# Performance work log

Hardware: AMD Instinct MI355X
Metric: run time of the kernel (lower is better)

Reference implementation:

```python
import jax, jax.numpy as jnp
import numpy as np
from jax import lax

BN_EPS = 1e-5


def _gate(x, w, g, b, m, v):
    """ZPool -> 7x7 conv (2->1 ch) -> BN (eval) -> sigmoid -> multiply. x: [B,C,H,W]."""
    z = jnp.concatenate(
        [x.max(axis=1, keepdims=True), x.mean(axis=1, keepdims=True)], axis=1
    )  # [B,2,H,W]
    y = lax.conv_general_dilated(
        z, w, window_strides=(1, 1), padding=((3, 3), (3, 3)),
        dimension_numbers=("NCHW", "OIHW", "NCHW"),
    )  # [B,1,H,W]
    y = (y - m) * lax.rsqrt(v + BN_EPS) * g + b
    return x * jax.nn.sigmoid(y)


def setup_inputs() -> dict:
    key = jax.random.key(0)
    ks = jax.random.split(key, 4)
    B, C, H, W = 32, 256, 56, 56
    return {
        "x": jax.random.normal(ks[0], (B, C, H, W), dtype=jnp.float32),
        "w_ch": jax.random.normal(ks[1], (1, 2, 7, 7), dtype=jnp.float32),
        "w_cw": jax.random.normal(ks[2], (1, 2, 7, 7), dtype=jnp.float32),
        "w_hw": jax.random.normal(ks[3], (1, 2, 7, 7), dtype=jnp.float32),
        "gamma": jnp.ones((3,), jnp.float32),
        "beta": jnp.zeros((3,), jnp.float32),
        "mean": jnp.zeros((3,), jnp.float32),
        "var": jnp.ones((3,), jnp.float32),
    }


def reference(x, w_ch, w_cw, w_hw, gamma, beta, mean, var):
    # Branch 1: swap C<->H -> gate -> swap back
    x_ch = jnp.transpose(x, (0, 2, 1, 3))
    x_ch = jnp.transpose(_gate(x_ch, w_ch, gamma[0], beta[0], mean[0], var[0]), (0, 2, 1, 3))
    # Branch 2: swap C<->W -> gate -> swap back
    x_cw = jnp.transpose(x, (0, 3, 2, 1))
    x_cw = jnp.transpose(_gate(x_cw, w_cw, gamma[1], beta[1], mean[1], var[1]), (0, 3, 2, 1))
    # Branch 3: identity spatial gate
    x_hw = _gate(x, w_hw, gamma[2], beta[2], mean[2], var[2])
    return (x_ch + x_cw + x_hw) / 3.0
```

## Files before the change

kernel.cpp:

```cpp
#include <hip/hip_runtime.h>
#include <math.h>


#define B_ 32
#define C_ 256
#define H_ 56
#define W_ 56
#define HW_ 3136
#define LDSW 60
#define CG 8
#define NGRP (C_ / CG)

__device__ __forceinline__ float4 f4max(float4 a, float4 b) {
    return make_float4(fmaxf(a.x, b.x), fmaxf(a.y, b.y), fmaxf(a.z, b.z), fmaxf(a.w, b.w));
}
__device__ __forceinline__ float4 f4add(float4 a, float4 b) {
    return make_float4(a.x + b.x, a.y + b.y, a.z + b.z, a.w + b.w);
}

__global__ __launch_bounds__(256) void pool_fused(const float* __restrict__ x,
                                                  float* __restrict__ P1,
                                                  float* __restrict__ P2,
                                                  float* __restrict__ P3p) {
    __shared__ float smem[H_ * LDSW];
    const int t = threadIdx.x;
    const int b = blockIdx.x >> 5;
    const int g = blockIdx.x & (NGRP - 1);
    const int c0 = g * CG;
    const float* __restrict__ base = x + (size_t)(b * C_ + c0) * HW_;

    const int s0 = t, s1i = t + 256, s2i = t + 512, s3i = t + 768;
    const int h0 = s0 / 14,  ad0 = h0 * LDSW + (s0 - h0 * 14) * 4;
    const int h1 = s1i / 14, ad1 = h1 * LDSW + (s1i - h1 * 14) * 4;
    const int h2 = s2i / 14, ad2 = h2 * LDSW + (s2i - h2 * 14) * 4;
    const int h3 = s3i / 14, ad3 = h3 * LDSW + (s3i - h3 * 14) * 4;

    float4 mx0, mx1, mx2, mx3, su0, su1, su2, su3;
    mx0 = mx1 = mx2 = mx3 = make_float4(-INFINITY, -INFINITY, -INFINITY, -INFINITY);
    su0 = su1 = su2 = su3 = make_float4(0.f, 0.f, 0.f, 0.f);

    const float4* bp = (const float4*)base;
    float4 cur0 = bp[s0], cur1 = bp[s1i], cur2 = bp[s2i];
    float4 cur3 = (t < 16) ? bp[s3i] : make_float4(0, 0, 0, 0);

    for (int cc = 0; cc < CG; ++cc) {
        float4 nx0, nx1, nx2, nx3;
        if (cc < CG - 1) {
            const float4* nb = (const float4*)(base + (size_t)(cc + 1) * HW_);
            nx0 = nb[s0]; nx1 = nb[s1i]; nx2 = nb[s2i];
            if (t < 16) nx3 = nb[s3i];
        }
        *(float4*)&smem[ad0] = cur0;
        *(float4*)&smem[ad1] = cur1;
        *(float4*)&smem[ad2] = cur2;
        if (t < 16) *(float4*)&smem[ad3] = cur3;
        mx0 = f4max(mx0, cur0); su0 = f4add(su0, cur0);
        mx1 = f4max(mx1, cur1); su1 = f4add(su1, cur1);
        mx2 = f4max(mx2, cur2); su2 = f4add(su2, cur2);
        if (t < 16) { mx3 = f4max(mx3, cur3); su3 = f4add(su3, cur3); }
        __syncthreads();

        const int c = c0 + cc;
        if (t < 224) {
            const int q = t & 3;
            {
                const int h = t >> 2;
                float m = -INFINITY, s = 0.f;
#pragma unroll
                for (int j = 0; j < 14; ++j) {
                    float v = smem[h * LDSW + q + 4 * j];
                    m = fmaxf(m, v); s += v;
                }
                m = fmaxf(m, __shfl_down(m, 1)); s += __shfl_down(s, 1);
                m = fmaxf(m, __shfl_down(m, 2)); s += __shfl_down(s, 2);
                if (q == 0) {
                    P2[(((size_t)b * 2 + 0) * H_ + h) * C_ + c] = m;
                    P2[(((size_t)b * 2 + 1) * H_ + h) * C_ + c] = s * (1.f / 56.f);
                }
            }
            {
                const int w = t >> 2;
                float m = -INFINITY, s = 0.f;
#pragma unroll
                for (int j = 0; j < 14; ++j) {
                    float v = smem[(q * 14 + j) * LDSW + w];
                    m = fmaxf(m, v); s += v;
                }
                m = fmaxf(m, __shfl_down(m, 1)); s += __shfl_down(s, 1);
                m = fmaxf(m, __shfl_down(m, 2)); s += __shfl_down(s, 2);
                if (q == 0) {
                    P1[(((size_t)b * 2 + 0) * C_ + c) * W_ + w] = m;
                    P1[(((size_t)b * 2 + 1) * C_ + c) * W_ + w] = s * (1.f / 56.f);
                }
            }
        }
        __syncthreads();
        if (cc < CG - 1) {
            cur0 = nx0; cur1 = nx1; cur2 = nx2;
            if (t < 16) cur3 = nx3;
        }
    }
    float4* Pm = (float4*)(P3p + ((size_t)(b * NGRP + g) * 2 + 0) * HW_);
    float4* Ps = (float4*)(P3p + ((size_t)(b * NGRP + g) * 2 + 1) * HW_);
    Pm[s0] = mx0; Pm[s1i] = mx1; Pm[s2i] = mx2;
    Ps[s0] = su0; Ps[s1i] = su1; Ps[s2i] = su2;
    if (t < 16) { Pm[s3i] = mx3; Ps[s3i] = su3; }
}

__global__ __launch_bounds__(256) void combine_p3(const float* __restrict__ P3p,
                                                  float* __restrict__ P3) {
    const int idx = blockIdx.x * 256 + threadIdx.x;
    const int b = idx / HW_;
    const int hw = idx - b * HW_;
    const float* src = P3p + (size_t)b * NGRP * 2 * HW_ + hw;
    float m = -INFINITY, s = 0.f;
#pragma unroll
    for (int gg = 0; gg < NGRP; ++gg) {
        m = fmaxf(m, src[(size_t)(2 * gg + 0) * HW_]);
        s += src[(size_t)(2 * gg + 1) * HW_];
    }
    P3[((size_t)b * 2 + 0) * HW_ + hw] = m;
    P3[((size_t)b * 2 + 1) * HW_ + hw] = s * (1.f / 256.f);
}

__global__ __launch_bounds__(256) void conv_all(const float* __restrict__ P1,
                                                const float* __restrict__ P2,
                                                const float* __restrict__ P3,
                                                const float* __restrict__ w_ch,
                                                const float* __restrict__ w_cw,
                                                const float* __restrict__ w_hw,
                                                const float* __restrict__ gamma,
                                                const float* __restrict__ beta,
                                                const float* __restrict__ mean,
                                                const float* __restrict__ var,
                                                float* __restrict__ s1,
                                                float* __restrict__ s2,
                                                float* __restrict__ s3) {
    const int k = blockIdx.z;
    const float* Z; const float* wsrc; float* S; int A, D;
    if (k == 0)      { Z = P1; wsrc = w_ch; S = s1; A = C_; D = W_; }
    else if (k == 1) { Z = P2; wsrc = w_cw; S = s2; A = H_; D = C_; }
    else             { Z = P3; wsrc = w_hw; S = s3; A = H_; D = W_; }

    __shared__ float wl[98];
    const int t = threadIdx.x;
    if (t < 98) wl[t] = wsrc[t];
    __syncthreads();

    const int b = blockIdx.y;
    const int AD = A * D;
    const int idx = blockIdx.x * 256 + t;
    if (idx >= AD) return;
    const int a = idx / D;
    const int d = idx - a * D;

    const float* Z0 = Z + (size_t)b * 2 * AD;
    float acc = 0.f;
#pragma unroll
    for (int dy = 0; dy < 7; ++dy) {
        int aa = a + dy - 3;
        if (aa < 0 || aa >= A) continue;
#pragma unroll
        for (int dx = 0; dx < 7; ++dx) {
            int dd = d + dx - 3;
            if (dd < 0 || dd >= D) continue;
            acc += Z0[aa * D + dd] * wl[dy * 7 + dx]
                 + Z0[AD + aa * D + dd] * wl[49 + dy * 7 + dx];
        }
    }
    float y = (acc - mean[k]) * rsqrtf(var[k] + 1e-5f) * gamma[k] + beta[k];
    S[(size_t)b * AD + idx] = 1.f / (1.f + expf(-y));
}

__global__ __launch_bounds__(256) void final_mul(const float* __restrict__ x,
                                                 const float* __restrict__ s1,
                                                 const float* __restrict__ s2,
                                                 const float* __restrict__ s3,
                                                 float* __restrict__ out) {
    const int vid = blockIdx.x * 256 + threadIdx.x;
    const int p = vid / 784;
    const int r = vid - p * 784;
    const int h = r / 14;
    const int w4 = (r - h * 14) << 2;
    const int b = p >> 8;
    const int c = p & 255;

    const size_t xoff = (size_t)p * HW_ + h * 56 + w4;
    const float4 xv = *(const float4*)(x + xoff);
    const float4 s1v = *(const float4*)(s1 + ((size_t)(b * C_ + c)) * W_ + w4);
    const float s2s = s2[((size_t)b * H_ + h) * C_ + c];
    const float4 s3v = *(const float4*)(s3 + ((size_t)b * H_ + h) * W_ + w4);

    float4 o;
    o.x = xv.x * (s1v.x + s2s + s3v.x) * (1.f / 3.f);
    o.y = xv.y * (s1v.y + s2s + s3v.y) * (1.f / 3.f);
    o.z = xv.z * (s1v.z + s2s + s3v.z) * (1.f / 3.f);
    o.w = xv.w * (s1v.w + s2s + s3v.w) * (1.f / 3.f);
    *(float4*)(out + xoff) = o;
}

extern "C" void kernel_launch(void* const* d_in, const int* in_sizes, int n_in,
                              void* d_out, int out_size, void* d_ws, size_t ws_size,
                              hipStream_t stream) {
    const float* x = (const float*)d_in[0];
    const float* w_ch = (const float*)d_in[1];
    const float* w_cw = (const float*)d_in[2];
    const float* w_hw = (const float*)d_in[3];
    const float* gamma = (const float*)d_in[4];
    const float* beta = (const float*)d_in[5];
    const float* mean = (const float*)d_in[6];
    const float* var = (const float*)d_in[7];
    float* out = (float*)d_out;

    float* ws = (float*)d_ws;
    float* P1 = ws;
    float* P2 = P1 + 917504;
    float* P3p = P2 + 917504;
    float* P3 = P3p + 6422528;
    float* s1 = P3 + 200704;
    float* s2 = s1 + 458752;
    float* s3 = s2 + 458752;

    pool_fused<<<B_ * NGRP, 256, 0, stream>>>(x, P1, P2, P3p);
    combine_p3<<<(B_ * HW_) / 256, 256, 0, stream>>>(P3p, P3);
    conv_all<<<dim3(56, B_, 3), 256, 0, stream>>>(P1, P2, P3, w_ch, w_cw, w_hw,
                                                  gamma, beta, mean, var, s1, s2, s3);
    final_mul<<<(B_ * C_ * HW_) / 4 / 256, 256, 0, stream>>>(x, s1, s2, s3, out);
}
```

Before: 265.6 us.

## Fuse channel-partial combine into conv kernel and double channel group size

```diff
diff --git a/kernel.cpp b/kernel.cpp
--- a/kernel.cpp
+++ b/kernel.cpp
@@ -8,7 +8,7 @@
 #define W_ 56
 #define HW_ 3136
 #define LDSW 60
-#define CG 8
+#define CG 16
 #define NGRP (C_ / CG)
 
 __device__ __forceinline__ float4 f4max(float4 a, float4 b) {
@@ -24,7 +24,7 @@
                                                   float* __restrict__ P3p) {
     __shared__ float smem[H_ * LDSW];
     const int t = threadIdx.x;
-    const int b = blockIdx.x >> 5;
+    const int b = blockIdx.x >> 4;
     const int g = blockIdx.x & (NGRP - 1);
     const int c0 = g * CG;
     const float* __restrict__ base = x + (size_t)(b * C_ + c0) * HW_;
@@ -107,25 +107,9 @@
     if (t < 16) { Pm[s3i] = mx3; Ps[s3i] = su3; }
 }
 
-__global__ __launch_bounds__(256) void combine_p3(const float* __restrict__ P3p,
-                                                  float* __restrict__ P3) {
-    const int idx = blockIdx.x * 256 + threadIdx.x;
-    const int b = idx / HW_;
-    const int hw = idx - b * HW_;
-    const float* src = P3p + (size_t)b * NGRP * 2 * HW_ + hw;
-    float m = -INFINITY, s = 0.f;
-#pragma unroll
-    for (int gg = 0; gg < NGRP; ++gg) {
-        m = fmaxf(m, src[(size_t)(2 * gg + 0) * HW_]);
-        s += src[(size_t)(2 * gg + 1) * HW_];
-    }
-    P3[((size_t)b * 2 + 0) * HW_ + hw] = m;
-    P3[((size_t)b * 2 + 1) * HW_ + hw] = s * (1.f / 256.f);
-}
-
 __global__ __launch_bounds__(256) void conv_all(const float* __restrict__ P1,
                                                 const float* __restrict__ P2,
-                                                const float* __restrict__ P3,
+                                                const float* __restrict__ P3p,
                                                 const float* __restrict__ w_ch,
                                                 const float* __restrict__ w_cw,
                                                 const float* __restrict__ w_hw,
@@ -136,18 +120,62 @@
                                                 float* __restrict__ s1,
                                                 float* __restrict__ s2,
                                                 float* __restrict__ s3) {
+    __shared__ float wl[98];
+    __shared__ float zmax[12 * 56];
+    __shared__ float zmean[12 * 56];
     const int k = blockIdx.z;
-    const float* Z; const float* wsrc; float* S; int A, D;
-    if (k == 0)      { Z = P1; wsrc = w_ch; S = s1; A = C_; D = W_; }
-    else if (k == 1) { Z = P2; wsrc = w_cw; S = s2; A = H_; D = C_; }
-    else             { Z = P3; wsrc = w_hw; S = s3; A = H_; D = W_; }
-
-    __shared__ float wl[98];
     const int t = threadIdx.x;
+    const int b = blockIdx.y;
+    const float* wsrc = (k == 0) ? w_ch : (k == 1) ? w_cw : w_hw;
     if (t < 98) wl[t] = wsrc[t];
+
+    if (k == 2) {
+        if (blockIdx.x >= 13) return;
+        const int i0 = blockIdx.x * 256;
+        const int alo = max(0, i0 / 56 - 3);
+        const int ahi = min(55, (i0 + 255) / 56 + 3);
+        const int nrows = ahi - alo + 1;
+        const float* src = P3p + (size_t)b * (NGRP * 2 * HW_);
+        for (int p = t; p < nrows * 56; p += 256) {
+            const int r = p / 56;
+            const int pos = (alo + r) * 56 + (p - r * 56);
+            float m = -INFINITY, s = 0.f;
+#pragma unroll
+            for (int g = 0; g < NGRP; ++g) {
+                m = fmaxf(m, src[(size_t)(2 * g + 0) * HW_ + pos]);
+                s += src[(size_t)(2 * g + 1) * HW_ + pos];
+            }
+            zmax[p] = m; zmean[p] = s * (1.f / 256.f);
+        }
+        __syncthreads();
+        const int idx = i0 + t;
+        if (idx < HW_) {
+            const int a = idx / 56, d = idx - a * 56;
+            float acc = 0.f;
+#pragma unroll
+            for (int dy = 0; dy < 7; ++dy) {
+                int aa = a + dy - 3;
+                if (aa < 0 || aa >= 56) continue;
+                const float* zm = &zmax[(aa - alo) * 56];
+                const float* zs = &zmean[(aa - alo) * 56];
+#pragma unroll
+                for (int dx = 0; dx < 7; ++dx) {
+                    int dd = d + dx - 3;
+                    if (dd < 0 || dd >= 56) continue;
+                    acc += zm[dd] * wl[dy * 7 + dx] + zs[dd] * wl[49 + dy * 7 + dx];
+                }
+            }
+            float y = (acc - mean[2]) * rsqrtf(var[2] + 1e-5f) * gamma[2] + beta[2];
+            s3[(size_t)b * HW_ + idx] = 1.f / (1.f + expf(-y));
+        }
+        return;
+    }
+
     __syncthreads();
-
-    const int b = blockIdx.y;
+    const float* Z; float* S; int A, D;
+    if (k == 0) { Z = P1; S = s1; A = C_; D = W_; }
+    else        { Z = P2; S = s2; A = H_; D = C_; }
+
     const int AD = A * D;
     const int idx = blockIdx.x * 256 + t;
     if (idx >= AD) return;
@@ -216,14 +244,12 @@
     float* P1 = ws;
     float* P2 = P1 + 917504;
     float* P3p = P2 + 917504;
-    float* P3 = P3p + 6422528;
-    float* s1 = P3 + 200704;
+    float* s1 = P3p + 3211264;
     float* s2 = s1 + 458752;
     float* s3 = s2 + 458752;
 
     pool_fused<<<B_ * NGRP, 256, 0, stream>>>(x, P1, P2, P3p);
-    combine_p3<<<(B_ * HW_) / 256, 256, 0, stream>>>(P3p, P3);
-    conv_all<<<dim3(56, B_, 3), 256, 0, stream>>>(P1, P2, P3, w_ch, w_cw, w_hw,
+    conv_all<<<dim3(56, B_, 3), 256, 0, stream>>>(P1, P2, P3p, w_ch, w_cw, w_hw,
                                                   gamma, beta, mean, var, s1, s2, s3);
     final_mul<<<(B_ * C_ * HW_) / 4 / 256, 256, 0, stream>>>(x, s1, s2, s3, out);
 }
```

Measured after the change: 262.1 us. About the same (-1.3%).
